# Kernel optimization log

Hardware: AMD Instinct MI355X
Metric: run time of the kernel (lower is better)

## Reference

```python
import jax, jax.numpy as jnp
import numpy as np

R, N, B, S = 20, 4096, 16, 256          # relations, total nodes, graphs, nodes per graph
DIN, HID, H = 512, 128, 4               # in_dim, hidden_dim, num_heads
D = HID * H                              # flattened node-feature width (=512)
E = 16384                                # edges per relation
NEG_SLOPE = 0.2


def _gat(h, src, dst, W, al, ar, b):
    # DGL GATConv, eval mode (dropout off), identity residual (in == H*out), allow_zero_in_degree
    z = (h @ W).reshape(N, H, HID)                        # [N,H,Dh]
    el = (z * al).sum(-1)                                 # [N,H]
    er = (z * ar).sum(-1)                                 # [N,H]
    e = jax.nn.leaky_relu(el[src] + er[dst], NEG_SLOPE)   # [E,H]
    m = jax.ops.segment_max(e, dst, num_segments=N)       # per-dst max (edge softmax)
    ex = jnp.exp(e - m[dst])
    den = jax.ops.segment_sum(ex, dst, num_segments=N)
    alpha = ex / den[dst]                                 # [E,H]
    agg = jax.ops.segment_sum(alpha[..., None] * z[src], dst, num_segments=N)
    return agg + h.reshape(N, H, HID) + b, alpha


def _rgat_conv(h, src, dst, W, al, ar, b):
    # HeteroGraphConv with aggregate='mean' over R relations; scan keeps memory flat
    def body(acc, xs):
        s, d, Wr, alr, arr, br = xs
        out, alpha = _gat(h, s, d, Wr, alr, arr, br)
        return acc + out, alpha.mean(-1)                  # attention meaned over heads -> [E]
    acc, attn = jax.lax.scan(body, jnp.zeros((N, H, HID), h.dtype), (src, dst, W, al, ar, b))
    return acc / R, attn                                  # [N,H,Dh], [R,E]


def setup_inputs() -> dict:
    key = jax.random.key(0)
    ks = jax.random.split(key, 24)
    f32 = jnp.float32
    p = lambda k, shape: jax.random.normal(k, shape, f32) * 0.05
    z = lambda shape: jnp.zeros(shape, f32)
    return {
        'feat': jax.random.normal(ks[0], (N, DIN), f32),
        'hyp_emb': jax.random.normal(ks[1], (B, D), f32),
        'edge_src': jax.random.randint(ks[2], (R, E), 0, N),
        'edge_dst': jax.random.randint(ks[3], (R, E), 0, N),
        'W1': p(ks[4], (R, DIN, H * HID)), 'al1': p(ks[5], (R, H, HID)), 'ar1': p(ks[6], (R, H, HID)), 'b1': z((R, H, HID)),
        'W2': p(ks[7], (R, D, H * HID)), 'al2': p(ks[8], (R, H, HID)), 'ar2': p(ks[9], (R, H, HID)), 'b2': z((R, H, HID)),
        'Wq': p(ks[10], (D, D)), 'bq': z(D), 'Wk': p(ks[11], (D, D)), 'bk': z(D),
        'Wv': p(ks[12], (D, D)), 'bv': z(D), 'Wo': p(ks[13], (D, D)), 'bo': z(D),
        'Wn1': p(ks[14], (2 * D, HID)), 'bn1': z(HID), 'Wn2': p(ks[15], (HID, 2)), 'bn2': z(2),
    }


def reference(feat, hyp_emb, edge_src, edge_dst,
              W1, al1, ar1, b1, W2, al2, ar2, b2,
              Wq, bq, Wk, bk, Wv, bv, Wo, bo, Wn1, bn1, Wn2, bn2):
    # --- RGAT (rgat_generation) layer 1 + attention weights ---
    h1, attn = _rgat_conv(feat, edge_src, edge_dst, W1, al1, ar1, b1)
    h1 = jax.nn.elu(h1.reshape(N, D))
    # --- layer 2 ---
    h2, _ = _rgat_conv(h1, edge_src, edge_dst, W2, al2, ar2, b2)
    feats = h2.reshape(N, D)
    # --- node importance: scatter-add edge attention onto dst nodes, summed over etypes ---
    imp = jax.ops.segment_sum(attn.reshape(-1), edge_dst.reshape(-1), num_segments=N)
    feats_p = feats.reshape(B, S, D)                      # uniform graphs: split+pad == reshape
    weighted = feats_p * imp.reshape(B, S)[..., None]
    # --- MultiheadAttention(embed=D, heads=4): query = hyp_emb broadcast to all S positions ---
    Hm, Dm = 4, D // 4
    q = (hyp_emb @ Wq + bq).reshape(B, Hm, 1, Dm)         # identical query at every position
    k = (feats_p @ Wk + bk).reshape(B, S, Hm, Dm).transpose(0, 2, 1, 3)
    v = (feats_p @ Wv + bv).reshape(B, S, Hm, Dm).transpose(0, 2, 1, 3)
    scores = jnp.einsum('bhqd,bhkd->bhqk', q, k) / jnp.sqrt(jnp.float32(Dm))
    a = jax.nn.softmax(scores, axis=-1)                   # [B,Hm,1,S]
    ctx = jnp.einsum('bhqk,bhkd->bhqd', a, v).reshape(B, 1, D)
    attn_out = jnp.broadcast_to(ctx @ Wo + bo, (B, S, D))
    # --- node classifier on concat(weighted feats, attention output) ---
    combined = jnp.concatenate([weighted, attn_out], axis=-1).reshape(N, 2 * D)
    node_logits = jax.nn.relu(combined @ Wn1 + bn1) @ Wn2 + bn2
    return node_logits, attn
```

## Files before the change

### kernel.cpp

```cpp
#include <hip/hip_runtime.h>
#include <hip/hip_bf16.h>
#include <math.h>

#define NREL 20
#define NN   4096
#define NE   16384
#define DF   512
#define NHD  4
#define DHH  128
#define NB   16
#define NS   256

typedef __attribute__((ext_vector_type(8))) __bf16 bf16x8;
typedef __attribute__((ext_vector_type(4))) float f32x4;

__device__ inline float bf2f(unsigned short u) {
    union { float f; unsigned int i; } c; c.i = ((unsigned int)u) << 16; return c.f;
}
__device__ inline unsigned short f2bu(float f) {
    union { __hip_bfloat16 b; unsigned short u; } c; c.b = __float2bfloat16(f); return c.u;
}
__device__ inline void storeOut(float* p, float v) { *p = v; }
__device__ inline void storeOut(__hip_bfloat16* p, float v) { *p = __float2bfloat16(v); }

__device__ inline void load_lds16(const __hip_bfloat16* g, __hip_bfloat16* l) {
    __builtin_amdgcn_global_load_lds(
        (const __attribute__((address_space(1))) unsigned int*)(const void*)g,
        (__attribute__((address_space(3))) unsigned int*)(void*)l, 16, 0, 0);
}

__device__ inline int kswz(int f, int row) { return f ^ ((((row) >> 1) & 3) << 3); }

__global__ __launch_bounds__(256) void prep_kernel(
    const float* __restrict__ feat, unsigned short* __restrict__ featbf,
    const float* __restrict__ b1, const float* __restrict__ b2,
    const float* __restrict__ bk, const float* __restrict__ bv,
    float* __restrict__ bsum1, float* __restrict__ bsum2,
    float* __restrict__ bkv, int* __restrict__ cnt, float* __restrict__ imp)
{
    int blk = blockIdx.x, t = threadIdx.x;
    if (blk < 1024) {
        int idx = blk * 256 + t;
        int row = idx >> 6;
        int f = (idx & 63) * 8;
        int fs = kswz(f, row);
        const float4* ip = (const float4*)&feat[(size_t)row * DF + f];
        float4 v0 = ip[0], v1 = ip[1];
        union { unsigned short u[8]; uint4 q; } o;
        o.u[0] = f2bu(v0.x); o.u[1] = f2bu(v0.y); o.u[2] = f2bu(v0.z); o.u[3] = f2bu(v0.w);
        o.u[4] = f2bu(v1.x); o.u[5] = f2bu(v1.y); o.u[6] = f2bu(v1.z); o.u[7] = f2bu(v1.w);
        *(uint4*)(featbf + (size_t)row * DF + fs) = o.q;
    } else if (blk == 1024) {
        #pragma unroll
        for (int rep = 0; rep < 2; ++rep) {
            int f = t + rep * 256;
            float s1 = 0.f, s2 = 0.f;
            #pragma unroll
            for (int r = 0; r < NREL; ++r) { s1 += b1[r * DF + f]; s2 += b2[r * DF + f]; }
            bsum1[f] = s1; bsum2[f] = s2;
        }
        for (int i = t; i < NN; i += 256) imp[i] = 0.f;
    } else if (blk == 1025) {
        #pragma unroll
        for (int j = 0; j < 4; ++j) {
            int f = t + j * 256;
            bkv[f] = (f < DF) ? bk[f] : bv[f - DF];
        }
    } else {
        int idx = (blk - 1026) * 256 + t;
        cnt[idx] = 0;
    }
}

__global__ void count_kernel(const int* __restrict__ dst, int* __restrict__ cnt) {
    int idx = blockIdx.x * 256 + threadIdx.x;
    int r = idx / NE;
    atomicAdd(&cnt[r * NN + dst[idx]], 1);
}

__global__ void scan_kernel(const int* __restrict__ cnt, int* __restrict__ rowptr,
                            int* __restrict__ woff, int* __restrict__ rowptr2) {
    int r = blockIdx.x;
    int t = threadIdx.x;
    __shared__ int sums[1024];
    int v[4]; int local = 0;
    if (r < NREL) {
        #pragma unroll
        for (int j = 0; j < 4; ++j) { v[j] = cnt[r * NN + t * 4 + j]; local += v[j]; }
    } else {
        #pragma unroll
        for (int j = 0; j < 4; ++j) {
            int s = 0;
            for (int rel = 0; rel < NREL; ++rel) s += cnt[rel * NN + t * 4 + j];
            v[j] = s; local += s;
        }
    }
    sums[t] = local;
    __syncthreads();
    for (int off = 1; off < 1024; off <<= 1) {
        int x = (t >= off) ? sums[t - off] : 0;
        __syncthreads();
        sums[t] += x;
        __syncthreads();
    }
    int run = (t == 0) ? 0 : sums[t - 1];
    if (r < NREL) {
        #pragma unroll
        for (int j = 0; j < 4; ++j) {
            rowptr[r * (NN + 1) + t * 4 + j] = run;
            woff[r * NN + t * 4 + j] = run;
            run += v[j];
        }
        if (t == 1023) rowptr[r * (NN + 1) + NN] = run;
    } else {
        #pragma unroll
        for (int j = 0; j < 4; ++j) { rowptr2[t * 4 + j] = run; run += v[j]; }
        if (t == 1023) rowptr2[NN] = run;
    }
}

__global__ void fill_kernel(const int* __restrict__ dst, const int* __restrict__ src,
                            int* __restrict__ woff, int* __restrict__ srcCSR,
                            int* __restrict__ eidCSR) {
    int idx = blockIdx.x * 256 + threadIdx.x;
    int r = idx / NE; int e = idx % NE;
    int pos = atomicAdd(&woff[r * NN + dst[idx]], 1);
    srcCSR[r * NE + pos] = src[idx];
    eidCSR[r * NE + pos] = e;
}

__global__ __launch_bounds__(256) void transw_kernel(
    const float* __restrict__ W, __hip_bfloat16* __restrict__ Wt, int K, int N)
{
    int r = blockIdx.z;
    __shared__ float t[32][33];
    int k0 = blockIdx.x * 32, n0 = blockIdx.y * 32;
    int tx = threadIdx.x % 32, ty = threadIdx.x / 32;
    #pragma unroll
    for (int kk = ty; kk < 32; kk += 8)
        t[kk][tx] = W[((size_t)r * K + k0 + kk) * N + n0 + tx];
    __syncthreads();
    #pragma unroll
    for (int nn = ty; nn < 32; nn += 8) {
        int row = n0 + nn;
        Wt[((size_t)r * N + row) * K + k0 + kswz(tx, row)] = __float2bfloat16(t[tx][nn]);
    }
}

__global__ __launch_bounds__(256) void transw_kv_kernel(
    const float* __restrict__ Wk, const float* __restrict__ Wv,
    __hip_bfloat16* __restrict__ Wt)
{
    int z = blockIdx.z;
    const float* W = z ? Wv : Wk;
    __shared__ float t[32][33];
    int k0 = blockIdx.x * 32, n0 = blockIdx.y * 32;
    int tx = threadIdx.x % 32, ty = threadIdx.x / 32;
    #pragma unroll
    for (int kk = ty; kk < 32; kk += 8)
        t[kk][tx] = W[(size_t)(k0 + kk) * DF + n0 + tx];
    __syncthreads();
    #pragma unroll
    for (int nn = ty; nn < 32; nn += 8) {
        int row = n0 + nn;
        Wt[((size_t)z * DF + row) * DF + k0 + kswz(tx, row)] = __float2bfloat16(t[tx][nn]);
    }
}

template <typename OutT, bool RELU, bool FUSE>
__global__ __launch_bounds__(256) void mfma_gemm(
    const __hip_bfloat16* __restrict__ A,
    const __hip_bfloat16* __restrict__ BtAll,
    const float* __restrict__ bias, int biasStride,
    OutT* __restrict__ Call, int M, int N, int K,
    const float* __restrict__ al, const float* __restrict__ ar,
    float* __restrict__ el, float* __restrict__ er)
{
    int r = blockIdx.z;
    const __hip_bfloat16* Bt = BtAll + (size_t)r * N * K;
    OutT* C = Call + (size_t)r * M * N;
    const int rowBase = blockIdx.y * 128;
    const int colBase = blockIdx.x * 128;
    __shared__ __hip_bfloat16 As[128 * 32];
    __shared__ __hip_bfloat16 Bs[128 * 32];
    const int tid = threadIdx.x;
    const int w = tid >> 6, l = tid & 63;
    const int wr = w >> 1, wc = w & 1;
    const int m15 = l & 15, q = l >> 4;
    const int sRow = w * 16 + (l >> 2);
    const int sK = (l & 3) * 8;
    const __hip_bfloat16* Ag0 = A + (size_t)(rowBase + sRow) * K + sK;
    const __hip_bfloat16* Ag1 = Ag0 + (size_t)64 * K;
    const __hip_bfloat16* Bg0 = Bt + (size_t)(colBase + sRow) * K + sK;
    const __hip_bfloat16* Bg1 = Bg0 + (size_t)64 * K;
    __hip_bfloat16* Asl0 = As + sRow * 32 + sK;
    __hip_bfloat16* Asl1 = Asl0 + 2048;
    __hip_bfloat16* Bsl0 = Bs + sRow * 32 + sK;
    __hip_bfloat16* Bsl1 = Bsl0 + 2048;
    const int swf = (m15 >> 1) & 3;

    f32x4 acc[4][4];
    #pragma unroll
    for (int i = 0; i < 4; ++i)
        #pragma unroll
        for (int j = 0; j < 4; ++j) acc[i][j] = (f32x4){0.f, 0.f, 0.f, 0.f};

    for (int k0 = 0; k0 < K; k0 += 32) {
        load_lds16(Ag0 + k0, Asl0);
        load_lds16(Ag1 + k0, Asl1);
        load_lds16(Bg0 + k0, Bsl0);
        load_lds16(Bg1 + k0, Bsl1);
        __syncthreads();
        bf16x8 a[4], b[4];
        #pragma unroll
        for (int i = 0; i < 4; ++i)
            a[i] = *(const bf16x8*)&As[(wr * 64 + i * 16 + m15) * 32 + (q ^ swf) * 8];
        #pragma unroll
        for (int j = 0; j < 4; ++j)
            b[j] = *(const bf16x8*)&Bs[(wc * 64 + j * 16 + m15) * 32 + (q ^ swf) * 8];
        #pragma unroll
        for (int i = 0; i < 4; ++i)
            #pragma unroll
            for (int j = 0; j < 4; ++j)
                acc[i][j] = __builtin_amdgcn_mfma_f32_16x16x32_bf16(a[i], b[j], acc[i][j], 0, 0, 0);
        __syncthreads();
    }

    #pragma unroll
    for (int i = 0; i < 4; ++i) {
        #pragma unroll
        for (int j = 0; j < 4; ++j) {
            int col = colBase + wc * 64 + j * 16 + m15;
            float bv = bias ? bias[r * biasStride + col] : 0.f;
            #pragma unroll
            for (int reg = 0; reg < 4; ++reg) {
                int row = rowBase + wr * 64 + i * 16 + q * 4 + reg;
                float v = acc[i][j][reg] + bv;
                if (RELU) v = fmaxf(v, 0.f);
                storeOut(&C[(size_t)row * N + col], v);
            }
        }
    }

    if (FUSE) {
        float alv[4], arv[4];
        #pragma unroll
        for (int j = 0; j < 4; ++j) {
            int col = colBase + wc * 64 + j * 16 + m15;
            alv[j] = al[r * DF + col];
            arv[j] = ar[r * DF + col];
        }
        float pe[4][4], pr[4][4];
        #pragma unroll
        for (int i = 0; i < 4; ++i)
            #pragma unroll
            for (int reg = 0; reg < 4; ++reg) {
                float se = 0.f, sr = 0.f;
                #pragma unroll
                for (int j = 0; j < 4; ++j) {
                    se += acc[i][j][reg] * alv[j];
                    sr += acc[i][j][reg] * arv[j];
                }
                pe[i][reg] = se; pr[i][reg] = sr;
            }
        #pragma unroll
        for (int off = 1; off < 16; off <<= 1)
            #pragma unroll
            for (int i = 0; i < 4; ++i)
                #pragma unroll
                for (int reg = 0; reg < 4; ++reg) {
                    pe[i][reg] += __shfl_xor(pe[i][reg], off);
                    pr[i][reg] += __shfl_xor(pr[i][reg], off);
                }
        float* eP = (float*)As;
        float* rP = eP + 256;
        if (m15 == 0) {
            #pragma unroll
            for (int i = 0; i < 4; ++i)
                #pragma unroll
                for (int reg = 0; reg < 4; ++reg) {
                    int rowL = wr * 64 + i * 16 + q * 4 + reg;
                    eP[rowL * 2 + wc] = pe[i][reg];
                    rP[rowL * 2 + wc] = pr[i][reg];
                }
        }
        __syncthreads();
        if (tid < 128) {
            int head = colBase >> 7;
            size_t idx = ((size_t)r * NN + rowBase + tid) * NHD + head;
            el[idx] = eP[tid * 2] + eP[tid * 2 + 1];
            er[idx] = rP[tid * 2] + rP[tid * 2 + 1];
        }
    }
}

template <typename OutT>
__global__ __launch_bounds__(256) void gemm_kernel(
    const float* __restrict__ A, const float* __restrict__ Bm,
    const float* __restrict__ bias, OutT* __restrict__ C,
    int M, int K, int Nn)
{
    int r = blockIdx.z;
    const float* B = Bm + (size_t)r * K * Nn;
    OutT* Cr = C + (size_t)r * M * Nn;
    int rowBase = blockIdx.y * 64;
    int colBase = blockIdx.x * 64;
    __shared__ float As[64][17];
    __shared__ float Bs[16][64];
    int tid = threadIdx.x;
    int tx = tid % 16, ty = tid / 16;
    float acc[4][4] = {};
    int aRow = tid / 4, aK4 = (tid % 4) * 4;
    int bK = tid / 16, bN4 = (tid % 16) * 4;
    for (int k0 = 0; k0 < K; k0 += 16) {
        int gRow = rowBase + aRow;
        float4 av = make_float4(0.f, 0.f, 0.f, 0.f);
        if (gRow < M) av = *(const float4*)(A + (size_t)gRow * K + k0 + aK4);
        As[aRow][aK4 + 0] = av.x; As[aRow][aK4 + 1] = av.y;
        As[aRow][aK4 + 2] = av.z; As[aRow][aK4 + 3] = av.w;
        float4 bv = *(const float4*)(B + (size_t)(k0 + bK) * Nn + colBase + bN4);
        *(float4*)&Bs[bK][bN4] = bv;
        __syncthreads();
        #pragma unroll
        for (int k = 0; k < 16; ++k) {
            float a[4], b[4];
            #pragma unroll
            for (int i = 0; i < 4; ++i) a[i] = As[ty * 4 + i][k];
            #pragma unroll
            for (int j = 0; j < 4; ++j) b[j] = Bs[k][tx * 4 + j];
            #pragma unroll
            for (int i = 0; i < 4; ++i)
                #pragma unroll
                for (int j = 0; j < 4; ++j) acc[i][j] += a[i] * b[j];
        }
        __syncthreads();
    }
    #pragma unroll
    for (int i = 0; i < 4; ++i) {
        int gRow = rowBase + ty * 4 + i;
        if (gRow >= M) continue;
        #pragma unroll
        for (int j = 0; j < 4; ++j) {
            int gCol = colBase + tx * 4 + j;
            float v = acc[i][j];
            if (bias) v += bias[gCol];
            storeOut(&Cr[(size_t)gRow * Nn + gCol], v);
        }
    }
}

__global__ __launch_bounds__(256) void alpha_kernel(
    const float* __restrict__ el, const float* __restrict__ er,
    const int* __restrict__ rowptr, const int* __restrict__ rowptr2,
    const int* __restrict__ cnt, const int* __restrict__ srcCSR,
    const int* __restrict__ eidCSR,
    float* __restrict__ alphaPk, int* __restrict__ srcPk,
    float* __restrict__ attn, float* __restrict__ imp)
{
    int t = blockIdx.x * 256 + threadIdx.x;
    int r = t / NN, n = t % NN;
    int start = rowptr[r * (NN + 1) + n];
    int d = rowptr[r * (NN + 1) + n + 1] - start;
    if (d == 0) return;
    float4 er4 = *(const float4*)&er[((size_t)r * NN + n) * NHD];
    float4 den = make_float4(0.f, 0.f, 0.f, 0.f);
    for (int j = 0; j < d; ++j) {
        int s = srcCSR[r * NE + start + j];
        float4 el4 = *(const float4*)&el[((size_t)r * NN + s) * NHD];
        float v0 = el4.x + er4.x; v0 = v0 > 0.f ? v0 : 0.2f * v0;
        float v1 = el4.y + er4.y; v1 = v1 > 0.f ? v1 : 0.2f * v1;
        float v2 = el4.z + er4.z; v2 = v2 > 0.f ? v2 : 0.2f * v2;
        float v3 = el4.w + er4.w; v3 = v3 > 0.f ? v3 : 0.2f * v3;
        den.x += __expf(v0); den.y += __expf(v1);
        den.z += __expf(v2); den.w += __expf(v3);
    }
    float4 inv = make_float4(1.f / den.x, 1.f / den.y, 1.f / den.z, 1.f / den.w);
    int pbase = rowptr2[n];
    for (int rp = 0; rp < r; ++rp) pbase += cnt[rp * NN + n];
    float impLoc = 0.f;
    for (int j = 0; j < d; ++j) {
        int s = srcCSR[r * NE + start + j];
        float4 el4 = *(const float4*)&el[((size_t)r * NN + s) * NHD];
        float v0 = el4.x + er4.x; v0 = v0 > 0.f ? v0 : 0.2f * v0;
        float v1 = el4.y + er4.y; v1 = v1 > 0.f ? v1 : 0.2f * v1;
        float v2 = el4.z + er4.z; v2 = v2 > 0.f ? v2 : 0.2f * v2;
        float v3 = el4.w + er4.w; v3 = v3 > 0.f ? v3 : 0.2f * v3;
        float4 a4 = make_float4(__expf(v0) * inv.x, __expf(v1) * inv.y,
                                __expf(v2) * inv.z, __expf(v3) * inv.w);
        *(float4*)&alphaPk[(size_t)(pbase + j) * 4] = a4;
        srcPk[pbase + j] = r * NN + s;
        if (attn) {
            float a = 0.25f * (a4.x + a4.y + a4.z + a4.w);
            attn[r * NE + eidCSR[r * NE + start + j]] = a;
            impLoc += a;
        }
    }
    if (attn) atomicAdd(&imp[n], impLoc);
}

__global__ __launch_bounds__(256) void aggc_kernel(
    const __hip_bfloat16* __restrict__ Z,
    const int* __restrict__ rowptr2, const int* __restrict__ srcPk,
    const float* __restrict__ alphaPk, const float* __restrict__ bsum,
    const float* __restrict__ hin, float* __restrict__ hout,
    __hip_bfloat16* __restrict__ hout_bf, int applyElu)
{
    int n = blockIdx.x;
    int w = threadIdx.x >> 6, lane = threadIdx.x & 63;
    int h = lane >> 4;
    int base = rowptr2[n];
    int deg = rowptr2[n + 1] - base;
    float acc[8] = {};
    int i = w * 2;
    int z0 = 0, z1 = 0; float a0 = 0.f, a1 = 0.f;
    if (i < deg)     { z0 = srcPk[base + i];     a0 = alphaPk[(size_t)(base + i) * 4 + h]; }
    if (i + 1 < deg) { z1 = srcPk[base + i + 1]; a1 = alphaPk[(size_t)(base + i + 1) * 4 + h]; }
    while (i < deg) {
        int cz0 = z0, cz1 = z1; float ca0 = a0, ca1 = a1;
        int ni = i + 8;
        if (ni < deg)     { z0 = srcPk[base + ni];     a0 = alphaPk[(size_t)(base + ni) * 4 + h]; }
        if (ni + 1 < deg) { z1 = srcPk[base + ni + 1]; a1 = alphaPk[(size_t)(base + ni + 1) * 4 + h]; }
        else a1 = 0.f;
        float4 r0 = *(const float4*)&Z[(size_t)cz0 * DF + lane * 8];
        float4 r1 = *(const float4*)&Z[(size_t)cz1 * DF + lane * 8];
        const unsigned short* u0 = (const unsigned short*)&r0;
        const unsigned short* u1 = (const unsigned short*)&r1;
        #pragma unroll
        for (int j = 0; j < 8; ++j) acc[j] += ca0 * bf2f(u0[j]) + ca1 * bf2f(u1[j]);
        i = ni;
    }
    __shared__ float red[4][DF];
    #pragma unroll
    for (int j = 0; j < 8; ++j) red[w][lane * 8 + j] = acc[j];
    __syncthreads();
    const float invR = 1.0f / NREL;
    const int sw = ((n >> 1) & 3) << 3;
    int f = threadIdx.x;
    #pragma unroll
    for (int rep = 0; rep < 2; ++rep, f += 256) {
        float v = red[0][f] + red[1][f] + red[2][f] + red[3][f];
        v = (v + bsum[f]) * invR + hin[(size_t)n * DF + f];
        if (applyElu) v = v > 0.f ? v : expm1f(v);
        hout[(size_t)n * DF + f] = v;
        hout_bf[(size_t)n * DF + (f ^ sw)] = __float2bfloat16(v);
    }
}

__global__ __launch_bounds__(256) void mha_scores(
    const float* __restrict__ q, const float* __restrict__ k,
    float* __restrict__ scores)
{
    int b = blockIdx.x;
    int w = threadIdx.x >> 6, lane = threadIdx.x & 63;
    int s = blockIdx.y * 4 + w;
    const float4* qp = (const float4*)&q[(size_t)b * DF + lane * 8];
    const float4* kp = (const float4*)&k[((size_t)(b * NS + s)) * DF + lane * 8];
    float4 q0 = qp[0], q1 = qp[1];
    float4 k0 = kp[0], k1 = kp[1];
    float p = q0.x * k0.x + q0.y * k0.y + q0.z * k0.z + q0.w * k0.w
            + q1.x * k1.x + q1.y * k1.y + q1.z * k1.z + q1.w * k1.w;
    #pragma unroll
    for (int off = 1; off < 16; off <<= 1) p += __shfl_xor(p, off);
    if ((lane & 15) == 0) {
        int h = lane >> 4;
        scores[((size_t)(b * NHD + h)) * NS + s] = p * 0.08838834764831845f;
    }
}

__global__ __launch_bounds__(256) void mha_soft(float* __restrict__ scores) {
    int b = blockIdx.x;
    int h = threadIdx.x >> 6, lane = threadIdx.x & 63;
    float* sp = &scores[((size_t)(b * NHD + h)) * NS];
    float v[4];
    float mx = -INFINITY;
    #pragma unroll
    for (int i = 0; i < 4; ++i) { v[i] = sp[lane + 64 * i]; mx = fmaxf(mx, v[i]); }
    #pragma unroll
    for (int off = 32; off; off >>= 1) mx = fmaxf(mx, __shfl_xor(mx, off));
    float sum = 0.f;
    #pragma unroll
    for (int i = 0; i < 4; ++i) { v[i] = __expf(v[i] - mx); sum += v[i]; }
    #pragma unroll
    for (int off = 32; off; off >>= 1) sum += __shfl_xor(sum, off);
    float inv = 1.0f / sum;
    #pragma unroll
    for (int i = 0; i < 4; ++i) sp[lane + 64 * i] = v[i] * inv;
}

__global__ __launch_bounds__(256) void mha_ctx(
    const float* __restrict__ scores, const float* __restrict__ v,
    float* __restrict__ ctx)
{
    int b = blockIdx.x, h = blockIdx.y;
    int t = threadIdx.x;
    int d = t & 127, half = t >> 7;
    __shared__ float a_s[NS];
    a_s[t] = scores[((size_t)(b * NHD + h)) * NS + t];
    __syncthreads();
    float acc = 0.f;
    const float* vp = &v[((size_t)(b * NS + half * 128)) * DF + h * DHH + d];
    #pragma unroll 4
    for (int i = 0; i < 128; ++i)
        acc += a_s[half * 128 + i] * vp[(size_t)i * DF];
    __shared__ float red[256];
    red[t] = acc;
    __syncthreads();
    if (t < 128) ctx[(size_t)b * DF + h * DHH + t] = red[t] + red[t + 128];
}

__global__ __launch_bounds__(256) void combined_kernel(
    const float* __restrict__ feats, const float* __restrict__ imp,
    const float* __restrict__ abuf, __hip_bfloat16* __restrict__ comb)
{
    int n = blockIdx.x;
    int t = threadIdx.x;
    int b = n >> 8;
    float im = imp[n];
    const int sw = ((n >> 1) & 3) << 3;
    #pragma unroll
    for (int rep = 0; rep < 4; ++rep) {
        int f = t + rep * 256;
        float v = (f < DF) ? feats[(size_t)n * DF + f] * im
                           : abuf[(size_t)b * DF + (f - DF)];
        comb[(size_t)n * (2 * DF) + (f ^ sw)] = __float2bfloat16(v);
    }
}

__global__ __launch_bounds__(256) void cls2_kernel(
    const float* __restrict__ hidden, const float* __restrict__ Wn2,
    const float* __restrict__ bn2, float* __restrict__ out)
{
    __shared__ float w2[256];
    int t = threadIdx.x;
    w2[t] = Wn2[t];
    __syncthreads();
    int n = blockIdx.x * 256 + t;
    const float* hp = &hidden[(size_t)n * 128];
    float p0 = bn2[0], p1 = bn2[1];
    #pragma unroll 4
    for (int kk = 0; kk < 128; ++kk) {
        float hv = hp[kk];
        p0 += hv * w2[kk * 2 + 0];
        p1 += hv * w2[kk * 2 + 1];
    }
    out[n * 2 + 0] = p0;
    out[n * 2 + 1] = p1;
}

extern "C" void kernel_launch(void* const* d_in, const int* in_sizes, int n_in,
                              void* d_out, int out_size, void* d_ws, size_t ws_size,
                              hipStream_t stream) {
    const float* feat = (const float*)d_in[0];
    const float* hyp  = (const float*)d_in[1];
    const int*   esrc = (const int*)d_in[2];
    const int*   edst = (const int*)d_in[3];
    const float* W1   = (const float*)d_in[4];
    const float* al1  = (const float*)d_in[5];
    const float* ar1  = (const float*)d_in[6];
    const float* b1   = (const float*)d_in[7];
    const float* W2   = (const float*)d_in[8];
    const float* al2  = (const float*)d_in[9];
    const float* ar2  = (const float*)d_in[10];
    const float* b2   = (const float*)d_in[11];
    const float* Wq = (const float*)d_in[12]; const float* bq = (const float*)d_in[13];
    const float* Wk = (const float*)d_in[14]; const float* bk = (const float*)d_in[15];
    const float* Wv = (const float*)d_in[16]; const float* bv = (const float*)d_in[17];
    const float* Wo = (const float*)d_in[18]; const float* bo = (const float*)d_in[19];
    const float* Wn1 = (const float*)d_in[20]; const float* bn1 = (const float*)d_in[21];
    const float* Wn2 = (const float*)d_in[22]; const float* bn2 = (const float*)d_in[23];

    char* ws = (char*)d_ws;
    size_t off = 0;
    auto alloc = [&](size_t bytes) -> void* {
        void* p = ws + off;
        off += (bytes + 255) & ~(size_t)255;
        return p;
    };
    __hip_bfloat16* Z = (__hip_bfloat16*)alloc((size_t)NREL * NN * DF * 2);
    float* el     = (float*)alloc((size_t)NREL * NN * NHD * 4);
    float* er     = (float*)alloc((size_t)NREL * NN * NHD * 4);
    int* rowptr   = (int*)alloc((size_t)NREL * (NN + 1) * 4);
    int* rowptr2  = (int*)alloc((size_t)(NN + 1) * 4);
    int* woff     = (int*)alloc((size_t)NREL * NN * 4);
    int* srcCSR   = (int*)alloc((size_t)NREL * NE * 4);
    int* eidCSR   = (int*)alloc((size_t)NREL * NE * 4);
    int* cnt      = (int*)alloc((size_t)NREL * NN * 4);
    int* srcPk    = (int*)alloc((size_t)NREL * NE * 4);
    float* alphaPk= (float*)alloc((size_t)NREL * NE * NHD * 4);
    float* bsum1  = (float*)alloc((size_t)DF * 4);
    float* bsum2  = (float*)alloc((size_t)DF * 4);
    float* bkv    = (float*)alloc((size_t)2 * DF * 4);
    float* h1     = (float*)alloc((size_t)NN * DF * 4);
    float* feats  = (float*)alloc((size_t)NN * DF * 4);
    float* imp    = (float*)alloc((size_t)NN * 4);
    float* kvbuf  = (float*)alloc((size_t)2 * NN * DF * 4);
    float* qbuf   = (float*)alloc((size_t)NB * DF * 4);
    float* ctxb   = (float*)alloc((size_t)NB * DF * 4);
    float* abuf   = (float*)alloc((size_t)NB * DF * 4);
    float* scoresb= (float*)alloc((size_t)NB * NHD * NS * 4);
    float* hidden = (float*)alloc((size_t)NN * 128 * 4);
    __hip_bfloat16* featbf  = (__hip_bfloat16*)alloc((size_t)NN * DF * 2);
    __hip_bfloat16* h1bf    = (__hip_bfloat16*)alloc((size_t)NN * DF * 2);
    __hip_bfloat16* featsbf = (__hip_bfloat16*)alloc((size_t)NN * DF * 2);
    __hip_bfloat16* combbf  = (__hip_bfloat16*)alloc((size_t)NN * 2 * DF * 2);
    __hip_bfloat16* Wt1 = (__hip_bfloat16*)alloc((size_t)NREL * DF * DF * 2);
    __hip_bfloat16* Wt2 = (__hip_bfloat16*)alloc((size_t)NREL * DF * DF * 2);
    __hip_bfloat16* WtKV = (__hip_bfloat16*)alloc((size_t)2 * DF * DF * 2);
    __hip_bfloat16* Wn1t = (__hip_bfloat16*)alloc((size_t)(2 * DF) * 128 * 2);
    if (off > ws_size) return;

    float* logits = (float*)d_out;
    float* attn   = (float*)d_out + (size_t)NN * 2;
    float* kbuf = kvbuf;
    float* vbuf = kvbuf + (size_t)NN * DF;

    prep_kernel<<<1026 + NREL * NN / 256, 256, 0, stream>>>(
        feat, (unsigned short*)featbf, b1, b2, bk, bv, bsum1, bsum2, bkv, cnt, imp);

    count_kernel<<<NREL * NE / 256, 256, 0, stream>>>(edst, cnt);
    scan_kernel<<<NREL + 1, 1024, 0, stream>>>(cnt, rowptr, woff, rowptr2);
    fill_kernel<<<NREL * NE / 256, 256, 0, stream>>>(edst, esrc, woff, srcCSR, eidCSR);

    transw_kernel<<<dim3(DF / 32, DF / 32, NREL), 256, 0, stream>>>(W1, Wt1, DF, DF);
    transw_kernel<<<dim3(DF / 32, DF / 32, NREL), 256, 0, stream>>>(W2, Wt2, DF, DF);
    transw_kv_kernel<<<dim3(DF / 32, DF / 32, 2), 256, 0, stream>>>(Wk, Wv, WtKV);
    transw_kernel<<<dim3(2 * DF / 32, 128 / 32, 1), 256, 0, stream>>>(Wn1, Wn1t, 2 * DF, 128);

    mfma_gemm<__hip_bfloat16, false, true><<<dim3(DF / 128, NN / 128, NREL), 256, 0, stream>>>(
        featbf, Wt1, nullptr, 0, Z, NN, DF, DF, al1, ar1, el, er);
    alpha_kernel<<<NREL * NN / 256, 256, 0, stream>>>(
        el, er, rowptr, rowptr2, cnt, srcCSR, eidCSR, alphaPk, srcPk, attn, imp);
    aggc_kernel<<<NN, 256, 0, stream>>>(Z, rowptr2, srcPk, alphaPk, bsum1,
                                        feat, h1, h1bf, 1);

    mfma_gemm<__hip_bfloat16, false, true><<<dim3(DF / 128, NN / 128, NREL), 256, 0, stream>>>(
        h1bf, Wt2, nullptr, 0, Z, NN, DF, DF, al2, ar2, el, er);
    alpha_kernel<<<NREL * NN / 256, 256, 0, stream>>>(
        el, er, rowptr, rowptr2, cnt, srcCSR, eidCSR, alphaPk, srcPk, nullptr, nullptr);
    aggc_kernel<<<NN, 256, 0, stream>>>(Z, rowptr2, srcPk, alphaPk, bsum2,
                                        h1, feats, featsbf, 0);

    mfma_gemm<float, false, false><<<dim3(DF / 128, NN / 128, 2), 256, 0, stream>>>(
        featsbf, WtKV, bkv, DF, kvbuf, NN, DF, DF, nullptr, nullptr, nullptr, nullptr);
    gemm_kernel<float><<<dim3(DF / 64, 1, 1), 256, 0, stream>>>(
        hyp, Wq, bq, qbuf, NB, DF, DF);
    mha_scores<<<dim3(NB, NS / 4), 256, 0, stream>>>(qbuf, kbuf, scoresb);
    mha_soft<<<NB, 256, 0, stream>>>(scoresb);
    mha_ctx<<<dim3(NB, NHD), 256, 0, stream>>>(scoresb, vbuf, ctxb);
    gemm_kernel<float><<<dim3(DF / 64, 1, 1), 256, 0, stream>>>(
        ctxb, Wo, bo, abuf, NB, DF, DF);

    combined_kernel<<<NN, 256, 0, stream>>>(feats, imp, abuf, combbf);
    mfma_gemm<float, true, false><<<dim3(1, NN / 128, 1), 256, 0, stream>>>(
        combbf, Wn1t, bn1, 0, hidden, NN, 128, 2 * DF, nullptr, nullptr, nullptr, nullptr);
    cls2_kernel<<<NN / 256, 256, 0, stream>>>(hidden, Wn2, bn2, logits);
}
```

Measured before the change: 641.2 us.

## Double GEMM K-tile to 64 with wider swizzle, precompute relation offsets, unroll gather

The MFMA GEMM now stages 64-wide K slices in LDS instead of 32. That halves the loop iterations and barriers, and the XOR swizzle changes to cover 8 chunks per row. Every producer of pre-swizzled bf16 layouts is updated to match. The scan kernel now precomputes per-relation prefix offsets (croff), so the alpha kernel no longer loops over earlier relations' counts. The aggregation gather loads four edges per warp per step with clamped indices, to raise memory-level parallelism. The cost is more LDS per block, which may lower occupancy, plus an extra buffer.

```diff
diff --git a/kernel.cpp b/kernel.cpp
--- a/kernel.cpp
+++ b/kernel.cpp
@@ -29,7 +29,7 @@
         (__attribute__((address_space(3))) unsigned int*)(void*)l, 16, 0, 0);
 }
 
-__device__ inline int kswz(int f, int row) { return f ^ ((((row) >> 1) & 3) << 3); }
+__device__ inline int kswz(int f, int row) { return f ^ (((row) & 7) << 3); }
 
 __global__ __launch_bounds__(256) void prep_kernel(
     const float* __restrict__ feat, unsigned short* __restrict__ featbf,
@@ -79,7 +79,8 @@
 }
 
 __global__ void scan_kernel(const int* __restrict__ cnt, int* __restrict__ rowptr,
-                            int* __restrict__ woff, int* __restrict__ rowptr2) {
+                            int* __restrict__ woff, int* __restrict__ rowptr2,
+                            int* __restrict__ croff) {
     int r = blockIdx.x;
     int t = threadIdx.x;
     __shared__ int sums[1024];
@@ -91,7 +92,10 @@
         #pragma unroll
         for (int j = 0; j < 4; ++j) {
             int s = 0;
-            for (int rel = 0; rel < NREL; ++rel) s += cnt[rel * NN + t * 4 + j];
+            for (int rel = 0; rel < NREL; ++rel) {
+                croff[rel * NN + t * 4 + j] = s;
+                s += cnt[rel * NN + t * 4 + j];
+            }
             v[j] = s; local += s;
         }
     }
@@ -143,7 +147,7 @@
     #pragma unroll
     for (int nn = ty; nn < 32; nn += 8) {
         int row = n0 + nn;
-        Wt[((size_t)r * N + row) * K + k0 + kswz(tx, row)] = __float2bfloat16(t[tx][nn]);
+        Wt[((size_t)r * N + row) * K + kswz(k0 + tx, row)] = __float2bfloat16(t[tx][nn]);
     }
 }
 
@@ -163,7 +167,7 @@
     #pragma unroll
     for (int nn = ty; nn < 32; nn += 8) {
         int row = n0 + nn;
-        Wt[((size_t)z * DF + row) * DF + k0 + kswz(tx, row)] = __float2bfloat16(t[tx][nn]);
+        Wt[((size_t)z * DF + row) * DF + kswz(k0 + tx, row)] = __float2bfloat16(t[tx][nn]);
     }
 }
 
@@ -181,23 +185,19 @@
     OutT* C = Call + (size_t)r * M * N;
     const int rowBase = blockIdx.y * 128;
     const int colBase = blockIdx.x * 128;
-    __shared__ __hip_bfloat16 As[128 * 32];
-    __shared__ __hip_bfloat16 Bs[128 * 32];
+    __shared__ __hip_bfloat16 As[128 * 64];
+    __shared__ __hip_bfloat16 Bs[128 * 64];
     const int tid = threadIdx.x;
     const int w = tid >> 6, l = tid & 63;
     const int wr = w >> 1, wc = w & 1;
     const int m15 = l & 15, q = l >> 4;
-    const int sRow = w * 16 + (l >> 2);
-    const int sK = (l & 3) * 8;
-    const __hip_bfloat16* Ag0 = A + (size_t)(rowBase + sRow) * K + sK;
-    const __hip_bfloat16* Ag1 = Ag0 + (size_t)64 * K;
-    const __hip_bfloat16* Bg0 = Bt + (size_t)(colBase + sRow) * K + sK;
-    const __hip_bfloat16* Bg1 = Bg0 + (size_t)64 * K;
-    __hip_bfloat16* Asl0 = As + sRow * 32 + sK;
-    __hip_bfloat16* Asl1 = Asl0 + 2048;
-    __hip_bfloat16* Bsl0 = Bs + sRow * 32 + sK;
-    __hip_bfloat16* Bsl1 = Bsl0 + 2048;
-    const int swf = (m15 >> 1) & 3;
+    const int sRow = tid >> 3;
+    const int sChk = tid & 7;
+    const __hip_bfloat16* Ag = A + (size_t)(rowBase + sRow) * K + sChk * 8;
+    const __hip_bfloat16* Bg = Bt + (size_t)(colBase + sRow) * K + sChk * 8;
+    __hip_bfloat16* Asl = As + tid * 8;
+    __hip_bfloat16* Bsl = Bs + tid * 8;
+    const int swr = m15 & 7;
 
     f32x4 acc[4][4];
     #pragma unroll
@@ -205,24 +205,28 @@
         #pragma unroll
         for (int j = 0; j < 4; ++j) acc[i][j] = (f32x4){0.f, 0.f, 0.f, 0.f};
 
-    for (int k0 = 0; k0 < K; k0 += 32) {
-        load_lds16(Ag0 + k0, Asl0);
-        load_lds16(Ag1 + k0, Asl1);
-        load_lds16(Bg0 + k0, Bsl0);
-        load_lds16(Bg1 + k0, Bsl1);
+    for (int k0 = 0; k0 < K; k0 += 64) {
+        #pragma unroll
+        for (int c = 0; c < 4; ++c) {
+            load_lds16(Ag + (size_t)c * 32 * K + k0, Asl + c * 2048);
+            load_lds16(Bg + (size_t)c * 32 * K + k0, Bsl + c * 2048);
+        }
         __syncthreads();
-        bf16x8 a[4], b[4];
-        #pragma unroll
-        for (int i = 0; i < 4; ++i)
-            a[i] = *(const bf16x8*)&As[(wr * 64 + i * 16 + m15) * 32 + (q ^ swf) * 8];
-        #pragma unroll
-        for (int j = 0; j < 4; ++j)
-            b[j] = *(const bf16x8*)&Bs[(wc * 64 + j * 16 + m15) * 32 + (q ^ swf) * 8];
-        #pragma unroll
-        for (int i = 0; i < 4; ++i)
+        #pragma unroll
+        for (int g = 0; g < 2; ++g) {
+            bf16x8 a[4], b[4];
+            #pragma unroll
+            for (int i = 0; i < 4; ++i)
+                a[i] = *(const bf16x8*)&As[(wr * 64 + i * 16 + m15) * 64 + ((g * 4 + q) ^ swr) * 8];
             #pragma unroll
             for (int j = 0; j < 4; ++j)
-                acc[i][j] = __builtin_amdgcn_mfma_f32_16x16x32_bf16(a[i], b[j], acc[i][j], 0, 0, 0);
+                b[j] = *(const bf16x8*)&Bs[(wc * 64 + j * 16 + m15) * 64 + ((g * 4 + q) ^ swr) * 8];
+            #pragma unroll
+            for (int i = 0; i < 4; ++i)
+                #pragma unroll
+                for (int j = 0; j < 4; ++j)
+                    acc[i][j] = __builtin_amdgcn_mfma_f32_16x16x32_bf16(a[i], b[j], acc[i][j], 0, 0, 0);
+        }
         __syncthreads();
     }
 
@@ -352,7 +356,7 @@
 __global__ __launch_bounds__(256) void alpha_kernel(
     const float* __restrict__ el, const float* __restrict__ er,
     const int* __restrict__ rowptr, const int* __restrict__ rowptr2,
-    const int* __restrict__ cnt, const int* __restrict__ srcCSR,
+    const int* __restrict__ croff, const int* __restrict__ srcCSR,
     const int* __restrict__ eidCSR,
     float* __restrict__ alphaPk, int* __restrict__ srcPk,
     float* __restrict__ attn, float* __restrict__ imp)
@@ -375,8 +379,7 @@
         den.z += __expf(v2); den.w += __expf(v3);
     }
     float4 inv = make_float4(1.f / den.x, 1.f / den.y, 1.f / den.z, 1.f / den.w);
-    int pbase = rowptr2[n];
-    for (int rp = 0; rp < r; ++rp) pbase += cnt[rp * NN + n];
+    int pbase = rowptr2[n] + croff[r * NN + n];
     float impLoc = 0.f;
     for (int j = 0; j < d; ++j) {
         int s = srcCSR[r * NE + start + j];
@@ -411,30 +414,45 @@
     int base = rowptr2[n];
     int deg = rowptr2[n + 1] - base;
     float acc[8] = {};
-    int i = w * 2;
-    int z0 = 0, z1 = 0; float a0 = 0.f, a1 = 0.f;
-    if (i < deg)     { z0 = srcPk[base + i];     a0 = alphaPk[(size_t)(base + i) * 4 + h]; }
-    if (i + 1 < deg) { z1 = srcPk[base + i + 1]; a1 = alphaPk[(size_t)(base + i + 1) * 4 + h]; }
-    while (i < deg) {
-        int cz0 = z0, cz1 = z1; float ca0 = a0, ca1 = a1;
-        int ni = i + 8;
-        if (ni < deg)     { z0 = srcPk[base + ni];     a0 = alphaPk[(size_t)(base + ni) * 4 + h]; }
-        if (ni + 1 < deg) { z1 = srcPk[base + ni + 1]; a1 = alphaPk[(size_t)(base + ni + 1) * 4 + h]; }
-        else a1 = 0.f;
-        float4 r0 = *(const float4*)&Z[(size_t)cz0 * DF + lane * 8];
-        float4 r1 = *(const float4*)&Z[(size_t)cz1 * DF + lane * 8];
-        const unsigned short* u0 = (const unsigned short*)&r0;
-        const unsigned short* u1 = (const unsigned short*)&r1;
-        #pragma unroll
-        for (int j = 0; j < 8; ++j) acc[j] += ca0 * bf2f(u0[j]) + ca1 * bf2f(u1[j]);
-        i = ni;
+    if (deg > 0) {
+        int i = w * 4;
+        int zz[4]; float aa[4];
+        #pragma unroll
+        for (int j = 0; j < 4; ++j) {
+            int idx = i + j; int cidx = idx < deg ? idx : deg - 1;
+            zz[j] = srcPk[base + cidx];
+            aa[j] = (idx < deg) ? alphaPk[(size_t)(base + cidx) * 4 + h] : 0.f;
+        }
+        while (i < deg) {
+            int cz[4]; float ca[4];
+            #pragma unroll
+            for (int j = 0; j < 4; ++j) { cz[j] = zz[j]; ca[j] = aa[j]; }
+            int ni = i + 16;
+            #pragma unroll
+            for (int j = 0; j < 4; ++j) {
+                int idx = ni + j; int cidx = idx < deg ? idx : deg - 1;
+                zz[j] = srcPk[base + cidx];
+                aa[j] = (idx < deg) ? alphaPk[(size_t)(base + cidx) * 4 + h] : 0.f;
+            }
+            float4 raw[4];
+            #pragma unroll
+            for (int j = 0; j < 4; ++j)
+                raw[j] = *(const float4*)&Z[(size_t)cz[j] * DF + lane * 8];
+            #pragma unroll
+            for (int j = 0; j < 4; ++j) {
+                const unsigned short* u = (const unsigned short*)&raw[j];
+                #pragma unroll
+                for (int e = 0; e < 8; ++e) acc[e] += ca[j] * bf2f(u[e]);
+            }
+            i = ni;
+        }
     }
     __shared__ float red[4][DF];
     #pragma unroll
     for (int j = 0; j < 8; ++j) red[w][lane * 8 + j] = acc[j];
     __syncthreads();
     const float invR = 1.0f / NREL;
-    const int sw = ((n >> 1) & 3) << 3;
+    const int sw = (n & 7) << 3;
     int f = threadIdx.x;
     #pragma unroll
     for (int rep = 0; rep < 2; ++rep, f += 256) {
@@ -516,7 +534,7 @@
     int t = threadIdx.x;
     int b = n >> 8;
     float im = imp[n];
-    const int sw = ((n >> 1) & 3) << 3;
+    const int sw = (n & 7) << 3;
     #pragma unroll
     for (int rep = 0; rep < 4; ++rep) {
         int f = t + rep * 256;
@@ -585,6 +603,7 @@
     int* srcCSR   = (int*)alloc((size_t)NREL * NE * 4);
     int* eidCSR   = (int*)alloc((size_t)NREL * NE * 4);
     int* cnt      = (int*)alloc((size_t)NREL * NN * 4);
+    int* croff    = (int*)alloc((size_t)NREL * NN * 4);
     int* srcPk    = (int*)alloc((size_t)NREL * NE * 4);
     float* alphaPk= (float*)alloc((size_t)NREL * NE * NHD * 4);
     float* bsum1  = (float*)alloc((size_t)DF * 4);
@@ -618,7 +637,7 @@
         feat, (unsigned short*)featbf, b1, b2, bk, bv, bsum1, bsum2, bkv, cnt, imp);
 
     count_kernel<<<NREL * NE / 256, 256, 0, stream>>>(edst, cnt);
-    scan_kernel<<<NREL + 1, 1024, 0, stream>>>(cnt, rowptr, woff, rowptr2);
+    scan_kernel<<<NREL + 1, 1024, 0, stream>>>(cnt, rowptr, woff, rowptr2, croff);
     fill_kernel<<<NREL * NE / 256, 256, 0, stream>>>(edst, esrc, woff, srcCSR, eidCSR);
 
     transw_kernel<<<dim3(DF / 32, DF / 32, NREL), 256, 0, stream>>>(W1, Wt1, DF, DF);
@@ -629,14 +648,14 @@
     mfma_gemm<__hip_bfloat16, false, true><<<dim3(DF / 128, NN / 128, NREL), 256, 0, stream>>>(
         featbf, Wt1, nullptr, 0, Z, NN, DF, DF, al1, ar1, el, er);
     alpha_kernel<<<NREL * NN / 256, 256, 0, stream>>>(
-        el, er, rowptr, rowptr2, cnt, srcCSR, eidCSR, alphaPk, srcPk, attn, imp);
+        el, er, rowptr, rowptr2, croff, srcCSR, eidCSR, alphaPk, srcPk, attn, imp);
     aggc_kernel<<<NN, 256, 0, stream>>>(Z, rowptr2, srcPk, alphaPk, bsum1,
                                         feat, h1, h1bf, 1);
 
     mfma_gemm<__hip_bfloat16, false, true><<<dim3(DF / 128, NN / 128, NREL), 256, 0, stream>>>(
         h1bf, Wt2, nullptr, 0, Z, NN, DF, DF, al2, ar2, el, er);
     alpha_kernel<<<NREL * NN / 256, 256, 0, stream>>>(
-        el, er, rowptr, rowptr2, cnt, srcCSR, eidCSR, alphaPk, srcPk, nullptr, nullptr);
+        el, er, rowptr, rowptr2, croff, srcCSR, eidCSR, alphaPk, srcPk, nullptr, nullptr);
     aggc_kernel<<<NN, 256, 0, stream>>>(Z, rowptr2, srcPk, alphaPk, bsum2,
                                         h1, feats, featsbf, 0);
 
```

Result: faster. 626.9 us (-2.2%).
